# Performance work log

Measured on AMD Instinct MI355X. Metric: run time of the kernel, lower is better.

## Reference

```python
import jax, jax.numpy as jnp
import numpy as np

N_NODES = 100000
N_EDGES = 640000
N_REL = 3
D_IN = 128
D_OUT = 128


def setup_inputs() -> dict:
    key = jax.random.key(0)
    ks = jax.random.split(key, 10)
    x = jax.random.normal(ks[0], (N_NODES, D_IN), dtype=jnp.float32)
    src = jax.random.randint(ks[1], (N_REL, N_EDGES), 0, N_NODES, dtype=jnp.int32)
    dst = jax.random.randint(ks[2], (N_REL, N_EDGES), 0, N_NODES, dtype=jnp.int32)
    s = 1.0 / np.sqrt(D_IN)
    W = jax.random.uniform(ks[3], (N_REL, D_IN, D_OUT), minval=-s, maxval=s, dtype=jnp.float32)
    b = jnp.zeros((N_REL, D_OUT), dtype=jnp.float32)
    sa = 1.0 / np.sqrt(D_OUT)
    Wa1 = jax.random.uniform(ks[4], (D_OUT, D_OUT), minval=-sa, maxval=sa, dtype=jnp.float32)
    ba1 = jax.random.uniform(ks[5], (D_OUT,), minval=-sa, maxval=sa, dtype=jnp.float32)
    wa2 = jax.random.uniform(ks[6], (D_OUT,), minval=-sa, maxval=sa, dtype=jnp.float32)
    return {"x": x, "src": src, "dst": dst, "W": W, "b": b,
            "Wa1": Wa1, "ba1": ba1, "wa2": wa2}


def _graph_conv(x, s, d, W_r, b_r, n):
    # DGL GraphConv, norm='both': D_out^{-1/2} -> W -> sum-aggregate -> D_in^{-1/2} -> +b
    ones = jnp.ones_like(s, dtype=x.dtype)
    deg_out = jnp.clip(jax.ops.segment_sum(ones, s, num_segments=n), 1.0)
    deg_in = jnp.clip(jax.ops.segment_sum(ones, d, num_segments=n), 1.0)
    h = (x * jax.lax.rsqrt(deg_out)[:, None]) @ W_r          # [N, D_out]
    agg = jax.ops.segment_sum(h[s], d, num_segments=n)        # gather + scatter-add
    return agg * jax.lax.rsqrt(deg_in)[:, None] + b_r


def reference(x, src, dst, W, b, Wa1, ba1, wa2):
    n = x.shape[0]
    # per-relation graph conv (loop over small fixed relation set)
    rel = jnp.stack([_graph_conv(x, src[r], dst[r], W[r], b[r], n)
                     for r in range(src.shape[0])])            # [R, N, D]
    # attention pooling over relation axis (softmax over dim 0)
    score = jnp.tanh(rel @ Wa1 + ba1) @ wa2                    # [R, N]
    attn = jax.nn.softmax(score, axis=0)[..., None]            # [R, N, 1]
    return (attn * rel).sum(axis=0)                            # [N, D]
```

## Files before the change

kernel.cpp:

```cpp
#include <hip/hip_runtime.h>

#define NN 100000
#define NE 640000
#define NR 3
#define DD 128
#define NSEG (NR * NN)
#define NBPR 782
#define NBUK (NR * NBPR)
#define BCAP 1280
#define CHUNK 8192
#define NBLK2 ((NR * NE + CHUNK - 1) / CHUNK)

typedef unsigned int u32;
typedef short bf8_t __attribute__((ext_vector_type(8)));
typedef float f4_t __attribute__((ext_vector_type(4)));

union U4 { uint4 u; bf8_t b; };

__device__ __forceinline__ u32 bfr(float f) {
  u32 u = __float_as_uint(f);
  return (u + 0x7fffu + ((u >> 16) & 1u)) >> 16;
}
__device__ __forceinline__ u32 packbf(float a, float b) {
  return bfr(a) | (bfr(b) << 16);
}
__device__ __forceinline__ float lo16(u32 u) { return __uint_as_float(u << 16); }
__device__ __forceinline__ float hi16(u32 u) { return __uint_as_float(u & 0xffff0000u); }
__device__ __forceinline__ float bf2f(u32 bits) { return __uint_as_float(bits << 16); }

__device__ __forceinline__ bf8_t ldfrag(const u32* p) {
  U4 t; t.u = *(const uint4*)p; return t.b;
}

__device__ __forceinline__ void gload_lds16(const u32* g, u32* l) {
  __builtin_amdgcn_global_load_lds((const __attribute__((address_space(1))) void*)g,
                                   (__attribute__((address_space(3))) void*)l, 16, 0, 0);
}

__global__ __launch_bounds__(256) void convert_x_kernel(const float* __restrict__ x,
                                                        u32* __restrict__ xb) {
  int i = blockIdx.x * 256 + threadIdx.x;
  if (i >= NN * 64) return;
  float2 v = ((const float2*)x)[i];
  xb[i] = packbf(v.x, v.y);
}

__global__ __launch_bounds__(512) void count_pass_kernel(const int* __restrict__ src,
                                                         const int* __restrict__ dst,
                                                         int* __restrict__ cnt_out,
                                                         int* __restrict__ cntmat) {
  __shared__ int cnt[NBUK];
  const int tid = threadIdx.x;
  for (int i = tid; i < NBUK; i += 512) cnt[i] = 0;
  __syncthreads();
  const int base = blockIdx.x * CHUNK;
  const int end = min(base + CHUNK, NR * NE);
  for (int i = base + tid; i < end; i += 512) {
    int r = i / NE;
    atomicAdd(&cnt_out[r * NN + src[i]], 1);
    atomicAdd(&cnt[r * NBPR + (dst[i] >> 7)], 1);
  }
  __syncthreads();
  for (int i = tid; i < NBUK; i += 512) cntmat[blockIdx.x * NBUK + i] = cnt[i];
}

__global__ __launch_bounds__(256) void rs_out_kernel(const int* __restrict__ cnt_out,
                                                     float* __restrict__ rs_out) {
  int i = blockIdx.x * 256 + threadIdx.x;
  if (i >= NSEG) return;
  int co = cnt_out[i]; if (co < 1) co = 1;
  rs_out[i] = rsqrtf((float)co);
}

__global__ __launch_bounds__(256) void scan_blocks_kernel(int* __restrict__ cntmat,
                                                          int* __restrict__ btot) {
  __shared__ int s[256];
  const int bk = blockIdx.x;
  const int t = threadIdx.x;
  int v = (t < NBLK2) ? cntmat[t * NBUK + bk] : 0;
  s[t] = v;
  __syncthreads();
  for (int d = 1; d < 256; d <<= 1) {
    int a = (t >= d) ? s[t - d] : 0;
    __syncthreads();
    s[t] += a;
    __syncthreads();
  }
  if (t < NBLK2) cntmat[t * NBUK + bk] = s[t] - v;
  if (t == 255) btot[bk] = s[255];
}

__global__ __launch_bounds__(256) void scan_buckets_kernel(const int* __restrict__ btot,
                                                           int* __restrict__ bucketbase) {
  __shared__ int s[256];
  const int tid = threadIdx.x;
  int v[10]; int loc = 0;
#pragma unroll
  for (int j = 0; j < 10; ++j) {
    int idx = tid * 10 + j;
    int c = (idx < NBUK) ? btot[idx] : 0;
    v[j] = c; loc += c;
  }
  s[tid] = loc;
  __syncthreads();
  for (int d = 1; d < 256; d <<= 1) {
    int t = (tid >= d) ? s[tid - d] : 0;
    __syncthreads();
    s[tid] += t;
    __syncthreads();
  }
  int run = s[tid] - loc;
#pragma unroll
  for (int j = 0; j < 10; ++j) {
    int idx = tid * 10 + j;
    if (idx < NBUK) bucketbase[idx] = run;
    run += v[j];
  }
  if (tid == 255) bucketbase[NBUK] = s[255];
}

__global__ __launch_bounds__(512) void place_pass_kernel(const int* __restrict__ src,
                                                         const int* __restrict__ dst,
                                                         const int* __restrict__ cntmat,
                                                         const int* __restrict__ bucketbase,
                                                         u32* __restrict__ bucketbuf) {
  __shared__ int cur[NBUK];
  const int tid = threadIdx.x;
  for (int i = tid; i < NBUK; i += 512)
    cur[i] = bucketbase[i] + cntmat[blockIdx.x * NBUK + i];
  __syncthreads();
  const int base = blockIdx.x * CHUNK;
  const int end = min(base + CHUNK, NR * NE);
  for (int i = base + tid; i < end; i += 512) {
    int r = i / NE;
    int d = dst[i];
    int bk = r * NBPR + (d >> 7);
    int pos = atomicAdd(&cur[bk], 1);
    bucketbuf[pos] = (u32)src[i] | ((u32)(d & 127) << 17);
  }
}

__global__ __launch_bounds__(256) void bucket_aggregate_kernel(
    const u32* __restrict__ xb, const u32* __restrict__ bucketbuf,
    const int* __restrict__ bucketbase, const float* __restrict__ rs_out,
    float* __restrict__ rs_in, u32* __restrict__ aggb) {
  __shared__ u32 eL[BCAP];
  __shared__ u32 sorted[BCAP];
  __shared__ int cntA[128], prefE[128], cur[128];
  const int tid = threadIdx.x;
  const int bk = blockIdx.x;
  const int r = bk / NBPR, bidx = bk % NBPR;
  const int node0 = bidx * 128;
  const int base = bucketbase[bk];
  const int count = min(bucketbase[bk + 1] - base, BCAP);
  if (tid < 128) cntA[tid] = 0;
  for (int i = tid; i < count; i += 256) eL[i] = bucketbuf[base + i];
  __syncthreads();
  for (int i = tid; i < count; i += 256) atomicAdd(&cntA[eL[i] >> 17], 1);
  __syncthreads();
  if (tid < 128) prefE[tid] = cntA[tid];
  __syncthreads();
  for (int d = 1; d < 128; d <<= 1) {
    int v = 0;
    if (tid < 128 && tid >= d) v = prefE[tid - d];
    __syncthreads();
    if (tid < 128) prefE[tid] += v;
    __syncthreads();
  }
  if (tid < 128) {
    int excl = prefE[tid] - cntA[tid];
    prefE[tid] = excl;
    cur[tid] = excl;
    int node = node0 + tid;
    if (node < NN) rs_in[r * NN + node] = rsqrtf((float)max(cntA[tid], 1));
  }
  __syncthreads();
  for (int i = tid; i < count; i += 256) {
    u32 v = eL[i];
    int pos = atomicAdd(&cur[v >> 17], 1);
    sorted[pos] = v & 0x1FFFFu;
  }
  __syncthreads();

  const int l16 = tid & 15, g = tid >> 4;
  const float* rsb = rs_out + r * NN;
  for (int nn = g; nn < 128; nn += 16) {
    const int node = node0 + nn;
    if (node >= NN) continue;
    const int beg = prefE[nn], cE = cntA[nn];
    float a[8] = {0.f, 0.f, 0.f, 0.f, 0.f, 0.f, 0.f, 0.f};
    int e = 0;
    for (; e + 1 < cE; e += 2) {
      int s0 = (int)sorted[beg + e], s1 = (int)sorted[beg + e + 1];
      float c0 = rsb[s0], c1 = rsb[s1];
      uint4 u0 = *(const uint4*)&xb[(size_t)s0 * 64 + l16 * 4];
      uint4 u1 = *(const uint4*)&xb[(size_t)s1 * 64 + l16 * 4];
      a[0] = fmaf(lo16(u0.x), c0, a[0]); a[1] = fmaf(hi16(u0.x), c0, a[1]);
      a[2] = fmaf(lo16(u0.y), c0, a[2]); a[3] = fmaf(hi16(u0.y), c0, a[3]);
      a[4] = fmaf(lo16(u0.z), c0, a[4]); a[5] = fmaf(hi16(u0.z), c0, a[5]);
      a[6] = fmaf(lo16(u0.w), c0, a[6]); a[7] = fmaf(hi16(u0.w), c0, a[7]);
      a[0] = fmaf(lo16(u1.x), c1, a[0]); a[1] = fmaf(hi16(u1.x), c1, a[1]);
      a[2] = fmaf(lo16(u1.y), c1, a[2]); a[3] = fmaf(hi16(u1.y), c1, a[3]);
      a[4] = fmaf(lo16(u1.z), c1, a[4]); a[5] = fmaf(hi16(u1.z), c1, a[5]);
      a[6] = fmaf(lo16(u1.w), c1, a[6]); a[7] = fmaf(hi16(u1.w), c1, a[7]);
    }
    if (e < cE) {
      int s0 = (int)sorted[beg + e];
      float c0 = rsb[s0];
      uint4 u0 = *(const uint4*)&xb[(size_t)s0 * 64 + l16 * 4];
      a[0] = fmaf(lo16(u0.x), c0, a[0]); a[1] = fmaf(hi16(u0.x), c0, a[1]);
      a[2] = fmaf(lo16(u0.y), c0, a[2]); a[3] = fmaf(hi16(u0.y), c0, a[3]);
      a[4] = fmaf(lo16(u0.z), c0, a[4]); a[5] = fmaf(hi16(u0.z), c0, a[5]);
      a[6] = fmaf(lo16(u0.w), c0, a[6]); a[7] = fmaf(hi16(u0.w), c0, a[7]);
    }
    uint4 o;
    o.x = packbf(a[0], a[1]);
    o.y = packbf(a[2], a[3]);
    o.z = packbf(a[4], a[5]);
    o.w = packbf(a[6], a[7]);
    *(uint4*)&aggb[((size_t)r * NN + node) * 64 + l16 * 4] = o;
  }
}

__global__ __launch_bounds__(256) void prep_wwa1_kernel(const float* __restrict__ W,
                                                        const float* __restrict__ Wa1,
                                                        float* __restrict__ WWa1) {
  int idx = blockIdx.x * 256 + threadIdx.x;
  if (idx >= NR * DD * DD) return;
  int r = idx >> 14, rem = idx & 16383, i = rem >> 7, c = rem & 127;
  const float* wrow = W + (r << 14) + (i << 7);
  float s = 0.f;
#pragma unroll 8
  for (int k = 0; k < DD; ++k) s = fmaf(wrow[k], Wa1[k * DD + c], s);
  WWa1[idx] = s;
}

__global__ __launch_bounds__(256) void prep_pack_kernel(const float* __restrict__ W,
                                                        const float* __restrict__ WWa1,
                                                        u32* __restrict__ wt_hi,
                                                        u32* __restrict__ wt_lo,
                                                        u32* __restrict__ wwt_hi) {
  int idx = blockIdx.x * 256 + threadIdx.x;
  if (idx >= NR * DD * 64) return;
  int r = idx >> 13, rem = idx & 8191, n = rem >> 6, ku = rem & 63;
  int k0 = ku * 2;
  {
    const float* M = W + (r << 14);
    float w0 = M[k0 * DD + n], w1 = M[(k0 + 1) * DD + n];
    u32 h0 = bfr(w0), h1 = bfr(w1);
    float l0 = w0 - bf2f(h0), l1 = w1 - bf2f(h1);
    wt_hi[idx] = h0 | (h1 << 16);
    wt_lo[idx] = packbf(l0, l1);
  }
  {
    const float* M = WWa1 + (r << 14);
    float w0 = M[k0 * DD + n], w1 = M[(k0 + 1) * DD + n];
    wwt_hi[idx] = bfr(w0) | (bfr(w1) << 16);
  }
}

__global__ __launch_bounds__(256) void prep_bsum_kernel(const float* __restrict__ b,
                                                        const float* __restrict__ Wa1,
                                                        const float* __restrict__ ba1,
                                                        float* __restrict__ bsum) {
  int idx = blockIdx.x * 256 + threadIdx.x;
  if (idx >= NR * DD) return;
  int r = idx >> 7, c = idx & 127;
  float s = ba1[c];
#pragma unroll 8
  for (int k = 0; k < DD; ++k) s = fmaf(b[r * DD + k], Wa1[k * DD + c], s);
  bsum[idx] = s;
}

#define MFMA(a, b, c) __builtin_amdgcn_mfma_f32_16x16x32_bf16((a), (b), (c), 0, 0, 0)

__global__ __launch_bounds__(256, 2) void score_pass_kernel(
    const u32* __restrict__ aggb, const u32* __restrict__ wwt_hi,
    const float* __restrict__ rs_in, const float* __restrict__ bsum,
    const float* __restrict__ wa2, float* __restrict__ evec,
    float* __restrict__ wvec) {
  __shared__ u32 As[8192];
  __shared__ u32 Bs[8192];
  __shared__ float scoreS[NR][2][128];
  const int tid = threadIdx.x;
  const int l = tid & 63, w = tid >> 6;
  const int wr = w >> 1, wc = w & 1;
  const int l15 = l & 15, lg = l >> 4;
  const int row0 = blockIdx.x * 128;

  float wa2v[4];
#pragma unroll
  for (int nf = 0; nf < 4; ++nf) wa2v[nf] = wa2[wc * 64 + nf * 16 + l15];

  for (int r = 0; r < NR; ++r) {
    if (r) __syncthreads();
    const u32* Ar = aggb + (size_t)r * NN * 64;
    const u32* Br = wwt_hi + (size_t)r * 8192;
#pragma unroll
    for (int it = 0; it < 8; ++it) {
      int s = it * 256 + tid;
      int row = s >> 4;
      int c = (s & 15) ^ (row & 7);
      int grow = min(row0 + row, NN - 1);
      gload_lds16(Ar + (size_t)grow * 64 + c * 4, &As[it * 1024 + w * 256]);
      gload_lds16(Br + row * 64 + c * 4, &Bs[it * 1024 + w * 256]);
    }
    __syncthreads();

    f4_t c2[4][4];
#pragma unroll
    for (int rf = 0; rf < 4; ++rf)
#pragma unroll
      for (int nf = 0; nf < 4; ++nf) c2[rf][nf] = (f4_t)0.f;

#pragma unroll
    for (int ks = 0; ks < 4; ++ks) {
      bf8_t a[4];
#pragma unroll
      for (int rf = 0; rf < 4; ++rf) {
        int m = wr * 64 + rf * 16 + l15;
        int ch = (ks * 4 + lg) ^ (m & 7);
        a[rf] = ldfrag(&As[m * 64 + ch * 4]);
      }
#pragma unroll
      for (int nf = 0; nf < 4; ++nf) {
        int n = wc * 64 + nf * 16 + l15;
        int ch = (ks * 4 + lg) ^ (n & 7);
        bf8_t bb = ldfrag(&Bs[n * 64 + ch * 4]);
#pragma unroll
        for (int rf = 0; rf < 4; ++rf) c2[rf][nf] = MFMA(a[rf], bb, c2[rf][nf]);
      }
    }

#pragma unroll
    for (int rf = 0; rf < 4; ++rf) {
      const int lr0 = wr * 64 + rf * 16 + lg * 4;
      float rsv[4];
#pragma unroll
      for (int reg = 0; reg < 4; ++reg)
        rsv[reg] = rs_in[r * NN + min(row0 + lr0 + reg, NN - 1)];
      float part[4] = {0.f, 0.f, 0.f, 0.f};
#pragma unroll
      for (int nf = 0; nf < 4; ++nf) {
        int col = wc * 64 + nf * 16 + l15;
        float bs = bsum[r * DD + col];
#pragma unroll
        for (int reg = 0; reg < 4; ++reg) {
          float t = fmaf(c2[rf][nf][reg], rsv[reg], bs);
          t = fminf(fmaxf(t, -15.f), 15.f);
          float ex = __expf(2.f * t);
          part[reg] = fmaf((ex - 1.f) / (ex + 1.f), wa2v[nf], part[reg]);
        }
      }
#pragma unroll
      for (int reg = 0; reg < 4; ++reg) {
        float p = part[reg];
        p += __shfl_xor(p, 1);
        p += __shfl_xor(p, 2);
        p += __shfl_xor(p, 4);
        p += __shfl_xor(p, 8);
        if (l15 == 0) scoreS[r][wc][lr0 + reg] = p;
      }
    }
  }
  __syncthreads();
  if (tid < 128) {
    int grow = row0 + tid;
    if (grow < NN) {
      float s0 = scoreS[0][0][tid] + scoreS[0][1][tid];
      float s1 = scoreS[1][0][tid] + scoreS[1][1][tid];
      float s2 = scoreS[2][0][tid] + scoreS[2][1][tid];
      float mx = fmaxf(s0, fmaxf(s1, s2));
      float e0 = __expf(s0 - mx), e1 = __expf(s1 - mx), e2 = __expf(s2 - mx);
      float inv = 1.f / (e0 + e1 + e2);
      e0 *= inv; e1 *= inv; e2 *= inv;
      evec[grow] = e0; evec[NN + grow] = e1; evec[2 * NN + grow] = e2;
      wvec[grow]          = e0 * rs_in[grow];
      wvec[NN + grow]     = e1 * rs_in[NN + grow];
      wvec[2 * NN + grow] = e2 * rs_in[2 * NN + grow];
    }
  }
}

__global__ __launch_bounds__(256, 2) void out_pass_kernel(
    const u32* __restrict__ aggb, const u32* __restrict__ wt_hi,
    const u32* __restrict__ wt_lo, const float* __restrict__ evec,
    const float* __restrict__ wvec, const float* __restrict__ bias,
    float* __restrict__ out) {
  __shared__ u32 As[8320];
  __shared__ u32 Bs[8192];
  __shared__ float eL[NR][128];
  __shared__ float wfL[NR][128];
  __shared__ float bL[NR][128];
  const int tid = threadIdx.x;
  const int l = tid & 63, w = tid >> 6;
  const int wr = w >> 1, wc = w & 1;
  const int l15 = l & 15, lg = l >> 4;
  const int row0 = blockIdx.x * 128;

  if (tid < 128) {
    int grow = min(row0 + tid, NN - 1);
#pragma unroll
    for (int r = 0; r < NR; ++r) {
      eL[r][tid]  = evec[r * NN + grow];
      wfL[r][tid] = wvec[r * NN + grow];
    }
  }
  for (int idx = tid; idx < NR * DD; idx += 256) bL[idx >> 7][idx & 127] = bias[idx];

  f4_t fo[4][4];

  for (int r = 0; r < NR; ++r) {
    if (r) __syncthreads();
    const u32* Ar = aggb + (size_t)r * NN * 64;
    const u32* Br = wt_hi + (size_t)r * 8192;
#pragma unroll
    for (int it = 0; it < 8; ++it) {
      int s = it * 256 + tid;
      int row = s >> 4;
      int c = (s & 15) ^ (row & 7);
      int grow = min(row0 + row, NN - 1);
      gload_lds16(Ar + (size_t)grow * 64 + c * 4, &As[it * 1024 + w * 256]);
      gload_lds16(Br + row * 64 + c * 4, &Bs[it * 1024 + w * 256]);
    }
    __syncthreads();

    if (r == 0) {
#pragma unroll
      for (int rf = 0; rf < 4; ++rf) {
        const int lr0 = wr * 64 + rf * 16 + lg * 4;
#pragma unroll
        for (int nf = 0; nf < 4; ++nf) {
          const int col = wc * 64 + nf * 16 + l15;
#pragma unroll
          for (int reg = 0; reg < 4; ++reg) {
            float v = eL[0][lr0 + reg] * bL[0][col];
            v = fmaf(eL[1][lr0 + reg], bL[1][col], v);
            v = fmaf(eL[2][lr0 + reg], bL[2][col], v);
            fo[rf][nf][reg] = v;
          }
        }
      }
    }

    f4_t cc[4][4];
#pragma unroll
    for (int rf = 0; rf < 4; ++rf)
#pragma unroll
      for (int nf = 0; nf < 4; ++nf) cc[rf][nf] = (f4_t)0.f;

#pragma unroll
    for (int ks = 0; ks < 4; ++ks) {
      bf8_t a[4];
#pragma unroll
      for (int rf = 0; rf < 4; ++rf) {
        int m = wr * 64 + rf * 16 + l15;
        int ch = (ks * 4 + lg) ^ (m & 7);
        a[rf] = ldfrag(&As[m * 64 + ch * 4]);
      }
#pragma unroll
      for (int nf = 0; nf < 4; ++nf) {
        int n = wc * 64 + nf * 16 + l15;
        int ch = (ks * 4 + lg) ^ (n & 7);
        bf8_t bh = ldfrag(&Bs[n * 64 + ch * 4]);
        bf8_t bl = ldfrag(wt_lo + (size_t)r * 8192 + n * 64 + (ks * 4 + lg) * 4);
#pragma unroll
        for (int rf = 0; rf < 4; ++rf) cc[rf][nf] = MFMA(a[rf], bh, cc[rf][nf]);
#pragma unroll
        for (int rf = 0; rf < 4; ++rf) cc[rf][nf] = MFMA(a[rf], bl, cc[rf][nf]);
      }
    }

#pragma unroll
    for (int rf = 0; rf < 4; ++rf) {
      const int lr0 = wr * 64 + rf * 16 + lg * 4;
#pragma unroll
      for (int nf = 0; nf < 4; ++nf)
#pragma unroll
        for (int reg = 0; reg < 4; ++reg)
          fo[rf][nf][reg] = fmaf(cc[rf][nf][reg], wfL[r][lr0 + reg], fo[rf][nf][reg]);
    }
  }

  __syncthreads();
  float* Asf = (float*)As;
  const int rloc = tid >> 2;
  const int c0 = (tid & 3) * 32;
#pragma unroll
  for (int half = 0; half < 2; ++half) {
    if (wr == half) {
#pragma unroll
      for (int rf = 0; rf < 4; ++rf)
#pragma unroll
        for (int nf = 0; nf < 4; ++nf)
#pragma unroll
          for (int reg = 0; reg < 4; ++reg)
            Asf[(rf * 16 + lg * 4 + reg) * 130 + wc * 64 + nf * 16 + l15] =
                fo[rf][nf][reg];
    }
    __syncthreads();
    int grow = row0 + half * 64 + rloc;
    if (grow < NN) {
#pragma unroll
      for (int j = 0; j < 8; ++j) {
        float4 v = *(const float4*)&Asf[rloc * 130 + c0 + j * 4];
        *(float4*)&out[(size_t)grow * DD + c0 + j * 4] = v;
      }
    }
    __syncthreads();
  }
}

extern "C" void kernel_launch(void* const* d_in, const int* in_sizes, int n_in,
                              void* d_out, int out_size, void* d_ws, size_t ws_size,
                              hipStream_t stream) {
  const float* x   = (const float*)d_in[0];
  const int*   src = (const int*)d_in[1];
  const int*   dst = (const int*)d_in[2];
  const float* W   = (const float*)d_in[3];
  const float* b   = (const float*)d_in[4];
  const float* Wa1 = (const float*)d_in[5];
  const float* ba1 = (const float*)d_in[6];
  const float* wa2 = (const float*)d_in[7];
  float* out = (float*)d_out;

  char* ws = (char*)d_ws;
  size_t off = 0;
  u32* aggb = (u32*)(ws + off); off += (size_t)NSEG * 64 * 4;
  u32* xb   = (u32*)(ws + off); off += (size_t)NN * 64 * 4;
  u32* bucketbuf = (u32*)(ws + off); off += (size_t)NR * NE * 4;
  int* cntmat  = (int*)(ws + off); off += (size_t)NBLK2 * NBUK * 4;
  int* cnt_out = (int*)(ws + off); off += (size_t)NSEG * 4;
  float* rs_out = (float*)(ws + off); off += (size_t)NSEG * 4;
  float* rs_in  = (float*)(ws + off); off += (size_t)NSEG * 4;
  float* evec   = (float*)(ws + off); off += (size_t)NSEG * 4;
  float* wvec   = (float*)(ws + off); off += (size_t)NSEG * 4;
  int* btot       = (int*)(ws + off); off += (size_t)NBUK * 4;
  int* bucketbase = (int*)(ws + off); off += (size_t)(NBUK + 4) * 4;
  float* WWa1  = (float*)(ws + off); off += (size_t)NR * DD * DD * 4;
  u32* wt_hi   = (u32*)(ws + off); off += (size_t)NR * DD * 64 * 4;
  u32* wt_lo   = (u32*)(ws + off); off += (size_t)NR * DD * 64 * 4;
  u32* wwt_hi  = (u32*)(ws + off); off += (size_t)NR * DD * 64 * 4;
  float* bsum  = (float*)(ws + off); off += (size_t)NR * DD * 4;
  if (ws_size < off) return;

  hipMemsetAsync(cnt_out, 0, (size_t)NSEG * 4, stream);

  prep_wwa1_kernel<<<(NR * DD * DD + 255) / 256, 256, 0, stream>>>(W, Wa1, WWa1);
  prep_pack_kernel<<<(NR * DD * 64 + 255) / 256, 256, 0, stream>>>(W, WWa1, wt_hi, wt_lo,
                                                                   wwt_hi);
  prep_bsum_kernel<<<(NR * DD + 255) / 256, 256, 0, stream>>>(b, Wa1, ba1, bsum);

  convert_x_kernel<<<(NN * 64 + 255) / 256, 256, 0, stream>>>(x, xb);
  count_pass_kernel<<<NBLK2, 512, 0, stream>>>(src, dst, cnt_out, cntmat);
  rs_out_kernel<<<(NSEG + 255) / 256, 256, 0, stream>>>(cnt_out, rs_out);
  scan_blocks_kernel<<<NBUK, 256, 0, stream>>>(cntmat, btot);
  scan_buckets_kernel<<<1, 256, 0, stream>>>(btot, bucketbase);
  place_pass_kernel<<<NBLK2, 512, 0, stream>>>(src, dst, cntmat, bucketbase, bucketbuf);
  bucket_aggregate_kernel<<<NBUK, 256, 0, stream>>>(xb, bucketbuf, bucketbase, rs_out,
                                                    rs_in, aggb);

  int gb = (NN + 127) / 128;
  score_pass_kernel<<<gb, 256, 0, stream>>>(aggb, wwt_hi, rs_in, bsum, wa2, evec, wvec);
  out_pass_kernel<<<gb, 256, 0, stream>>>(aggb, wt_hi, wt_lo, evec, wvec, b, out);
}
```

Baseline: 345.4 us.

## Fuse score and output passes into one kernel with online softmax

Merges the score and output GEMM kernels into one kernel that loads each aggregated tile once per relation. It computes both the attention score and the projected output from that tile, and accumulates unnormalized exp-weighted outputs with a running denominator. Weight fragments are now read straight from global memory in a repacked k-major layout instead of being staged in LDS. The row tile drops to 64 so LDS use and register pressure shrink. This removes a second full read of aggb, the evec/wvec round trip and one launch. In exchange it adds extra block barriers per relation, and softmax no longer subtracts the max (scores are bounded by the tanh clamp).

```diff
diff --git a/kernel.cpp b/kernel.cpp
--- a/kernel.cpp
+++ b/kernel.cpp
@@ -244,18 +244,19 @@
   if (idx >= NR * DD * 64) return;
   int r = idx >> 13, rem = idx & 8191, n = rem >> 6, ku = rem & 63;
   int k0 = ku * 2;
+  int oidx = (r << 13) + ((ku >> 2) << 9) + (n << 2) + (ku & 3);
   {
     const float* M = W + (r << 14);
     float w0 = M[k0 * DD + n], w1 = M[(k0 + 1) * DD + n];
     u32 h0 = bfr(w0), h1 = bfr(w1);
     float l0 = w0 - bf2f(h0), l1 = w1 - bf2f(h1);
-    wt_hi[idx] = h0 | (h1 << 16);
-    wt_lo[idx] = packbf(l0, l1);
+    wt_hi[oidx] = h0 | (h1 << 16);
+    wt_lo[oidx] = packbf(l0, l1);
   }
   {
     const float* M = WWa1 + (r << 14);
     float w0 = M[k0 * DD + n], w1 = M[(k0 + 1) * DD + n];
-    wwt_hi[idx] = bfr(w0) | (bfr(w1) << 16);
+    wwt_hi[oidx] = bfr(w0) | (bfr(w1) << 16);
   }
 }
 
@@ -274,71 +275,84 @@
 
 #define MFMA(a, b, c) __builtin_amdgcn_mfma_f32_16x16x32_bf16((a), (b), (c), 0, 0, 0)
 
-__global__ __launch_bounds__(256, 2) void score_pass_kernel(
-    const u32* __restrict__ aggb, const u32* __restrict__ wwt_hi,
-    const float* __restrict__ rs_in, const float* __restrict__ bsum,
-    const float* __restrict__ wa2, float* __restrict__ evec,
-    float* __restrict__ wvec) {
-  __shared__ u32 As[8192];
-  __shared__ u32 Bs[8192];
-  __shared__ float scoreS[NR][2][128];
+__global__ __launch_bounds__(256, 2) void tail_fused_kernel(
+    const u32* __restrict__ aggb, const u32* __restrict__ wt_hi,
+    const u32* __restrict__ wt_lo, const u32* __restrict__ wwt_hi,
+    const float* __restrict__ rs_in, const float* __restrict__ bias,
+    const float* __restrict__ bsum, const float* __restrict__ wa2,
+    float* __restrict__ out) {
+  __shared__ u32 As[4160];
+  __shared__ float scoreS[2][64];
+  __shared__ float eLs[64];
+  __shared__ float bL[NR][DD];
   const int tid = threadIdx.x;
   const int l = tid & 63, w = tid >> 6;
   const int wr = w >> 1, wc = w & 1;
   const int l15 = l & 15, lg = l >> 4;
-  const int row0 = blockIdx.x * 128;
+  const int row0 = blockIdx.x * 64;
+
+  for (int idx = tid; idx < NR * DD; idx += 256) bL[idx >> 7][idx & 127] = bias[idx];
 
   float wa2v[4];
 #pragma unroll
   for (int nf = 0; nf < 4; ++nf) wa2v[nf] = wa2[wc * 64 + nf * 16 + l15];
 
+  f4_t fo[2][4];
+  float denom[2][4];
+#pragma unroll
+  for (int rf = 0; rf < 2; ++rf)
+#pragma unroll
+    for (int reg = 0; reg < 4; ++reg) {
+      denom[rf][reg] = 0.f;
+#pragma unroll
+      for (int nf = 0; nf < 4; ++nf) fo[rf][nf][reg] = 0.f;
+    }
+
   for (int r = 0; r < NR; ++r) {
-    if (r) __syncthreads();
+    __syncthreads();
     const u32* Ar = aggb + (size_t)r * NN * 64;
-    const u32* Br = wwt_hi + (size_t)r * 8192;
-#pragma unroll
-    for (int it = 0; it < 8; ++it) {
+#pragma unroll
+    for (int it = 0; it < 4; ++it) {
       int s = it * 256 + tid;
       int row = s >> 4;
       int c = (s & 15) ^ (row & 7);
       int grow = min(row0 + row, NN - 1);
       gload_lds16(Ar + (size_t)grow * 64 + c * 4, &As[it * 1024 + w * 256]);
-      gload_lds16(Br + row * 64 + c * 4, &Bs[it * 1024 + w * 256]);
-    }
-    __syncthreads();
-
-    f4_t c2[4][4];
-#pragma unroll
-    for (int rf = 0; rf < 4; ++rf)
+    }
+    __syncthreads();
+
+    float rsv[2][4];
+#pragma unroll
+    for (int rf = 0; rf < 2; ++rf)
+#pragma unroll
+      for (int reg = 0; reg < 4; ++reg)
+        rsv[rf][reg] = rs_in[r * NN + min(row0 + wr * 32 + rf * 16 + lg * 4 + reg, NN - 1)];
+
+    f4_t c2[2][4];
+#pragma unroll
+    for (int rf = 0; rf < 2; ++rf)
 #pragma unroll
       for (int nf = 0; nf < 4; ++nf) c2[rf][nf] = (f4_t)0.f;
-
 #pragma unroll
     for (int ks = 0; ks < 4; ++ks) {
-      bf8_t a[4];
-#pragma unroll
-      for (int rf = 0; rf < 4; ++rf) {
-        int m = wr * 64 + rf * 16 + l15;
+      bf8_t a[2];
+#pragma unroll
+      for (int rf = 0; rf < 2; ++rf) {
+        int m = wr * 32 + rf * 16 + l15;
         int ch = (ks * 4 + lg) ^ (m & 7);
         a[rf] = ldfrag(&As[m * 64 + ch * 4]);
       }
 #pragma unroll
       for (int nf = 0; nf < 4; ++nf) {
         int n = wc * 64 + nf * 16 + l15;
-        int ch = (ks * 4 + lg) ^ (n & 7);
-        bf8_t bb = ldfrag(&Bs[n * 64 + ch * 4]);
-#pragma unroll
-        for (int rf = 0; rf < 4; ++rf) c2[rf][nf] = MFMA(a[rf], bb, c2[rf][nf]);
-      }
-    }
-
-#pragma unroll
-    for (int rf = 0; rf < 4; ++rf) {
-      const int lr0 = wr * 64 + rf * 16 + lg * 4;
-      float rsv[4];
-#pragma unroll
-      for (int reg = 0; reg < 4; ++reg)
-        rsv[reg] = rs_in[r * NN + min(row0 + lr0 + reg, NN - 1)];
+        bf8_t gb = ldfrag(wwt_hi + (size_t)r * 8192 + (ks * 4 + lg) * 512 + n * 4);
+#pragma unroll
+        for (int rf = 0; rf < 2; ++rf) c2[rf][nf] = MFMA(a[rf], gb, c2[rf][nf]);
+      }
+    }
+
+#pragma unroll
+    for (int rf = 0; rf < 2; ++rf) {
       float part[4] = {0.f, 0.f, 0.f, 0.f};
 #pragma unroll
       for (int nf = 0; nf < 4; ++nf) {
@@ -346,7 +360,7 @@
         float bs = bsum[r * DD + col];
 #pragma unroll
         for (int reg = 0; reg < 4; ++reg) {
-          float t = fmaf(c2[rf][nf][reg], rsv[reg], bs);
+          float t = fmaf(c2[rf][nf][reg], rsv[rf][reg], bs);
           t = fminf(fmaxf(t, -15.f), 15.f);
           float ex = __expf(2.f * t);
           part[reg] = fmaf((ex - 1.f) / (ex + 1.f), wa2v[nf], part[reg]);
@@ -359,150 +373,91 @@
         p += __shfl_xor(p, 2);
         p += __shfl_xor(p, 4);
         p += __shfl_xor(p, 8);
-        if (l15 == 0) scoreS[r][wc][lr0 + reg] = p;
-      }
-    }
-  }
-  __syncthreads();
-  if (tid < 128) {
-    int grow = row0 + tid;
-    if (grow < NN) {
-      float s0 = scoreS[0][0][tid] + scoreS[0][1][tid];
-      float s1 = scoreS[1][0][tid] + scoreS[1][1][tid];
-      float s2 = scoreS[2][0][tid] + scoreS[2][1][tid];
-      float mx = fmaxf(s0, fmaxf(s1, s2));
-      float e0 = __expf(s0 - mx), e1 = __expf(s1 - mx), e2 = __expf(s2 - mx);
-      float inv = 1.f / (e0 + e1 + e2);
-      e0 *= inv; e1 *= inv; e2 *= inv;
-      evec[grow] = e0; evec[NN + grow] = e1; evec[2 * NN + grow] = e2;
-      wvec[grow]          = e0 * rs_in[grow];
-      wvec[NN + grow]     = e1 * rs_in[NN + grow];
-      wvec[2 * NN + grow] = e2 * rs_in[2 * NN + grow];
-    }
-  }
-}
-
-__global__ __launch_bounds__(256, 2) void out_pass_kernel(
-    const u32* __restrict__ aggb, const u32* __restrict__ wt_hi,
-    const u32* __restrict__ wt_lo, const float* __restrict__ evec,
-    const float* __restrict__ wvec, const float* __restrict__ bias,
-    float* __restrict__ out) {
-  __shared__ u32 As[8320];
-  __shared__ u32 Bs[8192];
-  __shared__ float eL[NR][128];
-  __shared__ float wfL[NR][128];
-  __shared__ float bL[NR][128];
-  const int tid = threadIdx.x;
-  const int l = tid & 63, w = tid >> 6;
-  const int wr = w >> 1, wc = w & 1;
-  const int l15 = l & 15, lg = l >> 4;
-  const int row0 = blockIdx.x * 128;
-
-  if (tid < 128) {
-    int grow = min(row0 + tid, NN - 1);
-#pragma unroll
-    for (int r = 0; r < NR; ++r) {
-      eL[r][tid]  = evec[r * NN + grow];
-      wfL[r][tid] = wvec[r * NN + grow];
-    }
-  }
-  for (int idx = tid; idx < NR * DD; idx += 256) bL[idx >> 7][idx & 127] = bias[idx];
-
-  f4_t fo[4][4];
-
-  for (int r = 0; r < NR; ++r) {
-    if (r) __syncthreads();
-    const u32* Ar = aggb + (size_t)r * NN * 64;
-    const u32* Br = wt_hi + (size_t)r * 8192;
-#pragma unroll
-    for (int it = 0; it < 8; ++it) {
-      int s = it * 256 + tid;
-      int row = s >> 4;
-      int c = (s & 15) ^ (row & 7);
-      int grow = min(row0 + row, NN - 1);
-      gload_lds16(Ar + (size_t)grow * 64 + c * 4, &As[it * 1024 + w * 256]);
-      gload_lds16(Br + row * 64 + c * 4, &Bs[it * 1024 + w * 256]);
-    }
-    __syncthreads();
-
-    if (r == 0) {
-#pragma unroll
-      for (int rf = 0; rf < 4; ++rf) {
-        const int lr0 = wr * 64 + rf * 16 + lg * 4;
-#pragma unroll
-        for (int nf = 0; nf < 4; ++nf) {
-          const int col = wc * 64 + nf * 16 + l15;
-#pragma unroll
-          for (int reg = 0; reg < 4; ++reg) {
-            float v = eL[0][lr0 + reg] * bL[0][col];
-            v = fmaf(eL[1][lr0 + reg], bL[1][col], v);
-            v = fmaf(eL[2][lr0 + reg], bL[2][col], v);
-            fo[rf][nf][reg] = v;
-          }
-        }
-      }
-    }
-
-    f4_t cc[4][4];
-#pragma unroll
-    for (int rf = 0; rf < 4; ++rf)
-#pragma unroll
-      for (int nf = 0; nf < 4; ++nf) cc[rf][nf] = (f4_t)0.f;
-
+        if (l15 == 0) scoreS[wc][wr * 32 + rf * 16 + lg * 4 + reg] = p;
+      }
+    }
+    __syncthreads();
+    if (tid < 64) eLs[tid] = __expf(scoreS[0][tid] + scoreS[1][tid]);
+    __syncthreads();
+
+    float ev[2][4];
+#pragma unroll
+    for (int rf = 0; rf < 2; ++rf)
+#pragma unroll
+      for (int reg = 0; reg < 4; ++reg) {
+        ev[rf][reg] = eLs[wr * 32 + rf * 16 + lg * 4 + reg];
+        denom[rf][reg] += ev[rf][reg];
+      }
+
+    f4_t c1[2][4];
+#pragma unroll
+    for (int rf = 0; rf < 2; ++rf)
+#pragma unroll
+      for (int nf = 0; nf < 4; ++nf) c1[rf][nf] = (f4_t)0.f;
 #pragma unroll
     for (int ks = 0; ks < 4; ++ks) {
-      bf8_t a[4];
-#pragma unroll
-      for (int rf = 0; rf < 4; ++rf) {
-        int m = wr * 64 + rf * 16 + l15;
+      bf8_t a[2];
+#pragma unroll
+      for (int rf = 0; rf < 2; ++rf) {
+        int m = wr * 32 + rf * 16 + l15;
         int ch = (ks * 4 + lg) ^ (m & 7);
         a[rf] = ldfrag(&As[m * 64 + ch * 4]);
       }
 #pragma unroll
       for (int nf = 0; nf < 4; ++nf) {
         int n = wc * 64 + nf * 16 + l15;
-        int ch = (ks * 4 + lg) ^ (n & 7);
-        bf8_t bh = ldfrag(&Bs[n * 64 + ch * 4]);
-        bf8_t bl = ldfrag(wt_lo + (size_t)r * 8192 + n * 64 + (ks * 4 + lg) * 4);
-#pragma unroll
-        for (int rf = 0; rf < 4; ++rf) cc[rf][nf] = MFMA(a[rf], bh, cc[rf][nf]);
-#pragma unroll
-        for (int rf = 0; rf < 4; ++rf) cc[rf][nf] = MFMA(a[rf], bl, cc[rf][nf]);
-      }
-    }
-
-#pragma unroll
-    for (int rf = 0; rf < 4; ++rf) {
-      const int lr0 = wr * 64 + rf * 16 + lg * 4;
-#pragma unroll
-      for (int nf = 0; nf < 4; ++nf)
-#pragma unroll
-        for (int reg = 0; reg < 4; ++reg)
-          fo[rf][nf][reg] = fmaf(cc[rf][nf][reg], wfL[r][lr0 + reg], fo[rf][nf][reg]);
-    }
-  }
+        size_t bo = (size_t)r * 8192 + (ks * 4 + lg) * 512 + n * 4;
+        bf8_t bh = ldfrag(wt_hi + bo);
+        bf8_t bl = ldfrag(wt_lo + bo);
+#pragma unroll
+        for (int rf = 0; rf < 2; ++rf) c1[rf][nf] = MFMA(a[rf], bh, c1[rf][nf]);
+#pragma unroll
+        for (int rf = 0; rf < 2; ++rf) c1[rf][nf] = MFMA(a[rf], bl, c1[rf][nf]);
+      }
+    }
+
+#pragma unroll
+    for (int rf = 0; rf < 2; ++rf)
+#pragma unroll
+      for (int reg = 0; reg < 4; ++reg) {
+        float er = ev[rf][reg] * rsv[rf][reg];
+        float e = ev[rf][reg];
+#pragma unroll
+        for (int nf = 0; nf < 4; ++nf) {
+          int col = wc * 64 + nf * 16 + l15;
+          fo[rf][nf][reg] = fmaf(c1[rf][nf][reg], er, fo[rf][nf][reg]);
+          fo[rf][nf][reg] = fmaf(bL[r][col], e, fo[rf][nf][reg]);
+        }
+      }
+  }
+
+  float inv[2][4];
+#pragma unroll
+  for (int rf = 0; rf < 2; ++rf)
+#pragma unroll
+    for (int reg = 0; reg < 4; ++reg) inv[rf][reg] = 1.f / denom[rf][reg];
 
   __syncthreads();
   float* Asf = (float*)As;
-  const int rloc = tid >> 2;
-  const int c0 = (tid & 3) * 32;
+  const int rloc = tid >> 3;
+  const int c0 = (tid & 7) * 16;
 #pragma unroll
   for (int half = 0; half < 2; ++half) {
     if (wr == half) {
 #pragma unroll
-      for (int rf = 0; rf < 4; ++rf)
+      for (int rf = 0; rf < 2; ++rf)
 #pragma unroll
         for (int nf = 0; nf < 4; ++nf)
 #pragma unroll
           for (int reg = 0; reg < 4; ++reg)
             Asf[(rf * 16 + lg * 4 + reg) * 130 + wc * 64 + nf * 16 + l15] =
-                fo[rf][nf][reg];
-    }
-    __syncthreads();
-    int grow = row0 + half * 64 + rloc;
+                fo[rf][nf][reg] * inv[rf][reg];
+    }
+    __syncthreads();
+    int grow = row0 + half * 32 + rloc;
     if (grow < NN) {
 #pragma unroll
-      for (int j = 0; j < 8; ++j) {
+      for (int j = 0; j < 4; ++j) {
         float4 v = *(const float4*)&Asf[rloc * 130 + c0 + j * 4];
         *(float4*)&out[(size_t)grow * DD + c0 + j * 4] = v;
       }
@@ -533,8 +488,6 @@
   int* cnt_out = (int*)(ws + off); off += (size_t)NSEG * 4;
   float* rs_out = (float*)(ws + off); off += (size_t)NSEG * 4;
   float* rs_in  = (float*)(ws + off); off += (size_t)NSEG * 4;
-  float* evec   = (float*)(ws + off); off += (size_t)NSEG * 4;
-  float* wvec   = (float*)(ws + off); off += (size_t)NSEG * 4;
   int* btot       = (int*)(ws + off); off += (size_t)NBUK * 4;
   int* bucketbase = (int*)(ws + off); off += (size_t)(NBUK + 4) * 4;
   float* WWa1  = (float*)(ws + off); off += (size_t)NR * DD * DD * 4;
@@ -560,7 +513,6 @@
   bucket_aggregate_kernel<<<NBUK, 256, 0, stream>>>(xb, bucketbuf, bucketbase, rs_out,
                                                     rs_in, aggb);
 
-  int gb = (NN + 127) / 128;
-  score_pass_kernel<<<gb, 256, 0, stream>>>(aggb, wwt_hi, rs_in, bsum, wa2, evec, wvec);
-  out_pass_kernel<<<gb, 256, 0, stream>>>(aggb, wt_hi, wt_lo, evec, wvec, b, out);
-}
+  tail_fused_kernel<<<(NN + 63) / 64, 256, 0, stream>>>(aggb, wt_hi, wt_lo, wwt_hi,
+                                                        rs_in, b, bsum, wa2, out);
+}
```

Result: no change. 341.4 us (-1.2%).
